# Optimization experiments

Hardware: AMD Instinct MI355X
Metric: run time of the kernel (lower is better)

## Reference

```python
import jax, jax.numpy as jnp
import numpy as np

N = 200      # nodes (fixed by Linear(200,100) on x.T)
E = 8000     # edges
NFEAT, NHID, NCLASS = 8192, 2048, 512


def _cheb_conv(x, edge_index, edge_weight, W, b):
    """PyG ChebConv (K=3, sym norm, lambda_max=2): L_hat = -D^{-1/2} A D^{-1/2}.
    T0 = x, T1 = L_hat x, T2 = 2 L_hat T1 - T0; out = sum_k T_k @ W[k] + b."""
    row, col = edge_index[0], edge_index[1]
    deg = jax.ops.segment_sum(edge_weight, row, num_segments=N)
    safe = jnp.where(deg > 0, deg, 1.0)
    dinv = jnp.where(deg > 0, 1.0 / jnp.sqrt(safe), 0.0)
    norm = -dinv[row] * edge_weight * dinv[col]  # [E]

    def lap(z):  # messages from source j=row to target i=col
        return jax.ops.segment_sum(norm[:, None] * z[row], col, num_segments=N)

    T1 = lap(x)
    T2 = 2.0 * lap(T1) - x
    return x @ W[0] + T1 @ W[1] + T2 @ W[2] + b


def _forward_single(x, ei, ew, W1, b1, W2, b2):
    h = jax.nn.relu(_cheb_conv(x, ei, ew, W1, b1))
    # dropout is identity in eval mode
    return _cheb_conv(h, ei, ew, W2, b2)  # [N, NCLASS]


def _classifier(z, Wc1, bc1, Wc2, bc2, Wc3, bc3):
    h = jax.nn.relu(z @ Wc1.T + bc1)
    h = jax.nn.relu(h @ Wc2.T + bc2)
    return h @ Wc3.T + bc3  # [NCLASS, 1]


def setup_inputs() -> dict:
    key = jax.random.key(0)
    ks = jax.random.split(key, 12)
    inp = {
        'x1': jax.random.normal(ks[0], (N, NFEAT), jnp.float32),
        'edge_index1': jax.random.randint(ks[1], (2, E), 0, N, jnp.int64),
        'edge_attr1': jax.random.uniform(ks[2], (E,), jnp.float32),
        'x2': jax.random.normal(ks[3], (N, NFEAT), jnp.float32),
        'edge_index2': jax.random.randint(ks[4], (2, E), 0, N, jnp.int64),
        'edge_attr2': jax.random.uniform(ks[5], (E,), jnp.float32),
        'W1': jax.random.normal(ks[6], (3, NFEAT, NHID), jnp.float32) * (NFEAT ** -0.5),
        'b1': jnp.zeros((NHID,), jnp.float32),
        'W2': jax.random.normal(ks[7], (3, NHID, NCLASS), jnp.float32) * (NHID ** -0.5),
        'b2': jnp.zeros((NCLASS,), jnp.float32),
        'Wc1': jax.random.normal(ks[8], (100, 200), jnp.float32) * (200 ** -0.5),
        'bc1': jnp.zeros((100,), jnp.float32),
        'Wc2': jax.random.normal(ks[9], (50, 100), jnp.float32) * (100 ** -0.5),
        'bc2': jnp.zeros((50,), jnp.float32),
        'Wc3': jax.random.normal(ks[10], (1, 50), jnp.float32) * (50 ** -0.5),
        'bc3': jnp.zeros((1,), jnp.float32),
    }
    return inp


def reference(x1, edge_index1, edge_attr1, x2, edge_index2, edge_attr2,
              W1, b1, W2, b2, Wc1, bc1, Wc2, bc2, Wc3, bc3):
    o1 = _forward_single(x1, edge_index1, edge_attr1, W1, b1, W2, b2)
    o2 = _forward_single(x2, edge_index2, edge_attr2, W1, b1, W2, b2)
    out1 = _classifier(o1.T, Wc1, bc1, Wc2, bc2, Wc3, bc3)  # [NCLASS, 1]
    out2 = _classifier(o2.T, Wc1, bc1, Wc2, bc2, Wc3, bc3)
    return out1, out2
```

## Files before the change

kernel.cpp:

```cpp
#include <hip/hip_runtime.h>

typedef __attribute__((ext_vector_type(8))) short short8;
typedef __attribute__((ext_vector_type(4))) float f32x4;
typedef __attribute__((ext_vector_type(2))) float f32x2;
typedef __attribute__((ext_vector_type(4))) unsigned int u32x4;

#define NNODES 200
#define NEDGE  8000
#define NF1    8192
#define NH     2048
#define NCL    512
#define K1     24576
#define K2     6144
#define MR     512
#define MV     400
#define PV     400
#define KC1    16
#define BK1    1536
#define KC2    16
#define BK2    384

#define OFF_P1  0ull
#define SZ_P1   (16ull*PV*NH*4)
#define OFF_P2  (OFF_P1 + SZ_P1)
#define SZ_P2   (16ull*PV*NCL*4)
#define OFF_A1  (OFF_P2 + SZ_P2)
#define SZ_A1   ((unsigned long long)MR*K1*2)
#define OFF_A2  (OFF_A1 + SZ_A1)
#define SZ_A2   ((unsigned long long)MR*K2*2)
#define OFF_DEG (OFF_A2 + SZ_A2)
#define OFF_LD  (OFF_DEG + 2048)
#define OFF_LL  (OFF_LD + 320000ull)
#define OFF_Z   OFF_P1

static __device__ __forceinline__ unsigned short f2bf(float f) {
  unsigned int u = __float_as_uint(f);
  unsigned int r = (u + 0x7fffu + ((u >> 16) & 1u)) >> 16;
  return (unsigned short)r;
}
static __device__ __forceinline__ unsigned packbf(float a, float b) {
  return (unsigned)f2bf(a) | ((unsigned)f2bf(b) << 16);
}

__global__ void k_zero(f32x4* p1, int n1, f32x4* p2, int n2, f32x4* p3, int n3) {
  int i = blockIdx.x * 256 + threadIdx.x;
  f32x4 z = {0.f, 0.f, 0.f, 0.f};
  if (i < n1) p1[i] = z;
  i -= n1;
  if (i >= 0 && i < n2) p2[i] = z;
  i -= n2;
  if (i >= 0 && i < n3) p3[i] = z;
}

__global__ void k_deg(const int* __restrict__ ei1, const float* __restrict__ ew1,
                      const int* __restrict__ ei2, const float* __restrict__ ew2,
                      float* __restrict__ deg) {
  int e = blockIdx.x * 256 + threadIdx.x;
  if (e >= 2 * NEDGE) return;
  int g = e / NEDGE, k = e % NEDGE;
  const int* ei = g ? ei2 : ei1;
  const float* ew = g ? ew2 : ew1;
  atomicAdd(deg + g * NNODES + ei[k], ew[k]);
}

__global__ void k_buildL(const int* __restrict__ ei1, const float* __restrict__ ew1,
                         const int* __restrict__ ei2, const float* __restrict__ ew2,
                         const float* __restrict__ deg, float* __restrict__ Ld) {
  int e = blockIdx.x * 256 + threadIdx.x;
  if (e >= 2 * NEDGE) return;
  int g = e / NEDGE, k = e % NEDGE;
  const int* ei = g ? ei2 : ei1;
  const float* ew = g ? ew2 : ew1;
  int r = ei[k], c = ei[NEDGE + k];
  float dr = deg[g * NNODES + r], dc = deg[g * NNODES + c];
  float ir = dr > 0.f ? 1.0f / sqrtf(dr) : 0.f;
  float ic = dc > 0.f ? 1.0f / sqrtf(dc) : 0.f;
  float nrm = -ir * ew[k] * ic;
  atomicAdd(Ld + ((size_t)g * NNODES + c) * NNODES + r, nrm);
}

__global__ void k_LL(const float* __restrict__ Ld, unsigned short* __restrict__ LLb) {
  int b = blockIdx.x;
  int g = b / NNODES, i = b % NNODES;
  __shared__ float Lr[NNODES];
  const float* Lg = Ld + (size_t)g * NNODES * NNODES;
  int t = threadIdx.x;
  if (t < NNODES) Lr[t] = Lg[i * NNODES + t];
  __syncthreads();
  if (t < NNODES) {
    float acc = 0.f;
    for (int k = 0; k < NNODES; ++k) acc = fmaf(Lr[k], Lg[k * NNODES + t], acc);
    unsigned short* LLg = LLb + (size_t)g * MR * 224;
    LLg[(size_t)i * 224 + t] = f2bf(Lr[t]);
    LLg[(size_t)(NNODES + i) * 224 + t] = f2bf(2.f * acc - (i == t ? 1.f : 0.f));
  }
}

__global__ void k_t0(const float* __restrict__ x1, const float* __restrict__ x2,
                     unsigned short* __restrict__ A1) {
  int gid = blockIdx.x * 256 + threadIdx.x;
  int row = gid / (NF1 / 8);
  int c8 = (gid % (NF1 / 8)) * 8;
  const float* xp = (row < NNODES ? x1 + (size_t)row * NF1
                                  : x2 + (size_t)(row - NNODES) * NF1) + c8;
  f32x4 a = *(const f32x4*)xp;
  f32x4 b = *(const f32x4*)(xp + 4);
  u32x4 o;
  o[0] = packbf(a[0], a[1]);
  o[1] = packbf(a[2], a[3]);
  o[2] = packbf(b[0], b[1]);
  o[3] = packbf(b[2], b[3]);
  *(u32x4*)(A1 + (size_t)row * K1 + c8) = o;
}

__global__ __launch_bounds__(256, 1)
void k_abuild(const unsigned short* __restrict__ LLb, const unsigned short* __restrict__ Asrc,
              unsigned short* __restrict__ Adst, const int Nf, const int Ka) {
  __shared__ __align__(16) unsigned short XF[7][4][64][8];
  const int g = blockIdx.x & 1;
  const int nt = blockIdx.x >> 1;
  const int nbase = nt * 64;
  const int t = threadIdx.x;

  #pragma unroll
  for (int it = 0; it < 14; ++it) {
    const int pos = it * 256 + t;
    const int j = pos >> 4;
    const int n4 = (pos & 15) * 4;
    unsigned long long v = 0ull;
    if (j < NNODES)
      v = *(const unsigned long long*)(Asrc + (size_t)(g * NNODES + j) * Ka + nbase + n4);
    const int ks = j >> 5, kg = (j >> 3) & 3, jj = j & 7;
    #pragma unroll
    for (int e = 0; e < 4; ++e) {
      const int nn = n4 + e;
      XF[ks][nn >> 4][(nn & 15) + 16 * kg][jj] = (unsigned short)(v >> (16 * e));
    }
  }
  __syncthreads();

  const int w = t >> 6, lane = t & 63;
  const int lm = lane & 15, lk8 = (lane >> 4) * 8;
  f32x4 acc[7][4];
  #pragma unroll
  for (int i = 0; i < 7; ++i)
    #pragma unroll
    for (int j = 0; j < 4; ++j) acc[i][j] = (f32x4){0.f, 0.f, 0.f, 0.f};

  const unsigned short* LLg = LLb + (size_t)g * MR * 224;
  #pragma unroll
  for (int ks = 0; ks < 7; ++ks) {
    short8 bfr[4];
    #pragma unroll
    for (int nf = 0; nf < 4; ++nf) bfr[nf] = *(const short8*)&XF[ks][nf][lane][0];
    short8 af[7];
    #pragma unroll
    for (int mf = 0; mf < 7; ++mf)
      af[mf] = *(const short8*)(LLg + (size_t)(w * 112 + mf * 16 + lm) * 224 + ks * 32 + lk8);
    #pragma unroll
    for (int mf = 0; mf < 7; ++mf)
      #pragma unroll
      for (int nf = 0; nf < 4; ++nf)
        acc[mf][nf] = __builtin_amdgcn_mfma_f32_16x16x32_bf16(af[mf], bfr[nf], acc[mf][nf], 0, 0, 0);
  }

  const int lr4 = (lane >> 4) * 4;
  #pragma unroll
  for (int mf = 0; mf < 7; ++mf) {
    #pragma unroll
    for (int ri = 0; ri < 4; ++ri) {
      const int m = w * 112 + mf * 16 + lr4 + ri;
      if (m < MV) {
        const int drow = g * NNODES + (m < NNODES ? m : m - NNODES);
        const size_t dbase = (size_t)drow * Ka + (m < NNODES ? Nf : 2 * Nf) + nbase + lm;
        #pragma unroll
        for (int nf = 0; nf < 4; ++nf)
          Adst[dbase + nf * 16] = f2bf(acc[mf][nf][ri]);
      }
    }
  }
}

template <int BN>
__global__ __launch_bounds__(512, 2)
void k_gemm(const float* __restrict__ W, const unsigned short* __restrict__ A,
            float* __restrict__ P, const int Nn, const int BK, const int Ka) {
  constexpr int NF = BN / 16;
  constexpr int NFW = BN / 32;
  __shared__ __align__(16) unsigned short Atile[MR * 64];
  __shared__ __align__(16) unsigned short Wt[2 * NF * 64 * 8];

  const int t = threadIdx.x;
  const int w = t >> 6, lane = t & 63;
  const int wm = w >> 1, wn = w & 1;
  const int lm = lane & 15;
  const int l4 = lane >> 4;
  const int kc = blockIdx.x & 15;
  const int nt = blockIdx.x >> 4;
  const int kbase = kc * BK;
  const int nbase = nt * BN;
  const int nks = BK >> 6;

  int offAg[8];
  int offAl[8];
  #pragma unroll
  for (int c = 0; c < 8; ++c) {
    const int off = c * 8192 + t * 16;
    const int row = off >> 7;
    const int rb = off & 127;
    const int gb = rb ^ ((row & 7) << 4);
    offAg[c] = row * (Ka * 2) + gb;
    offAl[c] = off;
  }
  const char* Ab = (const char*)A + (size_t)kbase * 2;

  constexpr int RW = (BN == 128) ? 4 : 2;
  constexpr int CW = (BN == 128) ? 4 : 2;
  const int kk0 = (BN == 128) ? ((t >> 5) * 4) : ((t >> 4) * 2);
  const int colb = (BN == 128) ? ((t & 31) * 4) : ((t & 15) * 2);
  int offWg[RW];
  #pragma unroll
  for (int r = 0; r < RW; ++r)
    offWg[r] = (kbase + kk0 + r) * Nn + nbase + colb;
  int offWl[RW / 2][CW];
  #pragma unroll
  for (int pr = 0; pr < RW / 2; ++pr) {
    const int kk = kk0 + 2 * pr;
    const int ks = kk >> 5, kg = (kk >> 3) & 3, jj1 = (kk & 7) >> 1;
    #pragma unroll
    for (int e = 0; e < CW; ++e) {
      const int nn = colb + e;
      const int nf = nn >> 4;
      const int ln = ((nn & 15) + 16 * kg) ^ (nf & 3);
      offWl[pr][e] = ((ks * NF + nf) * 64 + ln) * 4 + jj1;
    }
  }

  int aAddr[8];
  #pragma unroll
  for (int mf = 0; mf < 8; ++mf) {
    const int row = wm * 128 + mf * 16 + lm;
    aAddr[mf] = row * 128 + ((l4 * 16) ^ ((row & 7) << 4));
  }
  int bAddr[NFW];
  #pragma unroll
  for (int nf = 0; nf < NFW; ++nf) {
    const int nfg = wn * NFW + nf;
    bAddr[nf] = ((nfg * 64) + (lane ^ (nfg & 3))) * 16;
  }
  constexpr int BSTRIDE = NF * 64 * 16;

  f32x4 acc[8][NFW];
  #pragma unroll
  for (int i = 0; i < 8; ++i)
    #pragma unroll
    for (int j = 0; j < NFW; ++j) acc[i][j] = (f32x4){0.f, 0.f, 0.f, 0.f};

  u32x4 areg[8];
  f32x4 wv4[RW];
  f32x2 wv2[RW];

  #pragma unroll
  for (int c = 0; c < 8; ++c) areg[c] = *(const u32x4*)(Ab + offAg[c]);
  #pragma unroll
  for (int r = 0; r < RW; ++r) {
    if constexpr (BN == 128) wv4[r] = __builtin_nontemporal_load((const f32x4*)(W + offWg[r]));
    else                     wv2[r] = __builtin_nontemporal_load((const f32x2*)(W + offWg[r]));
  }
  {
    #pragma unroll
    for (int c = 0; c < 8; ++c) *(u32x4*)((char*)Atile + offAl[c]) = areg[c];
    unsigned* w32 = (unsigned*)Wt;
    #pragma unroll
    for (int pr = 0; pr < RW / 2; ++pr)
      #pragma unroll
      for (int e = 0; e < CW; ++e) {
        float lo = (BN == 128) ? wv4[2 * pr][e] : wv2[2 * pr][e];
        float hi = (BN == 128) ? wv4[2 * pr + 1][e] : wv2[2 * pr + 1][e];
        w32[offWl[pr][e]] = packbf(lo, hi);
      }
  }
  __syncthreads();

  for (int kt = 0; kt < nks; ++kt) {
    const bool more = (kt + 1 < nks);
    if (more) {
      const int ko = (kt + 1) * 128;
      #pragma unroll
      for (int c = 0; c < 8; ++c) areg[c] = *(const u32x4*)(Ab + offAg[c] + ko);
      const size_t kwo = (size_t)(kt + 1) * 64 * Nn;
      #pragma unroll
      for (int r = 0; r < RW; ++r) {
        if constexpr (BN == 128) wv4[r] = __builtin_nontemporal_load((const f32x4*)(W + offWg[r] + kwo));
        else                     wv2[r] = __builtin_nontemporal_load((const f32x2*)(W + offWg[r] + kwo));
      }
    }
    #pragma unroll
    for (int ks = 0; ks < 2; ++ks) {
      short8 bfr[NFW];
      #pragma unroll
      for (int nf = 0; nf < NFW; ++nf)
        bfr[nf] = *(const short8*)((const char*)Wt + bAddr[nf] + ks * BSTRIDE);
      short8 af[8];
      #pragma unroll
      for (int mf = 0; mf < 8; ++mf)
        af[mf] = *(const short8*)((const char*)Atile + (aAddr[mf] ^ (ks * 64)));
      #pragma unroll
      for (int mf = 0; mf < 8; ++mf)
        #pragma unroll
        for (int nf = 0; nf < NFW; ++nf)
          acc[mf][nf] = __builtin_amdgcn_mfma_f32_16x16x32_bf16(af[mf], bfr[nf], acc[mf][nf], 0, 0, 0);
    }
    __syncthreads();
    if (more) {
      #pragma unroll
      for (int c = 0; c < 8; ++c) *(u32x4*)((char*)Atile + offAl[c]) = areg[c];
      unsigned* w32 = (unsigned*)Wt;
      #pragma unroll
      for (int pr = 0; pr < RW / 2; ++pr)
        #pragma unroll
        for (int e = 0; e < CW; ++e) {
          float lo = (BN == 128) ? wv4[2 * pr][e] : wv2[2 * pr][e];
          float hi = (BN == 128) ? wv4[2 * pr + 1][e] : wv2[2 * pr + 1][e];
          w32[offWl[pr][e]] = packbf(lo, hi);
        }
    }
    __syncthreads();
  }

  float* Pk = P + ((size_t)kc * PV) * Nn + nbase;
  #pragma unroll
  for (int mf = 0; mf < 8; ++mf) {
    const int row0 = wm * 128 + mf * 16 + l4 * 4;
    #pragma unroll
    for (int ri = 0; ri < 4; ++ri) {
      const int row = row0 + ri;
      if (row < MV) {
        #pragma unroll
        for (int nf = 0; nf < NFW; ++nf) {
          const int col = (wn * NFW + nf) * 16 + lm;
          __builtin_nontemporal_store(acc[mf][nf][ri], Pk + (size_t)row * Nn + col);
        }
      }
    }
  }
}

__global__ void k_ep1(const float* __restrict__ P1, const float* __restrict__ b1,
                      unsigned short* __restrict__ A2) {
  int gid = blockIdx.x * 256 + threadIdx.x;
  int row = gid / (NH / 4);
  int c = (gid % (NH / 4)) * 4;
  f32x4 s = {0.f, 0.f, 0.f, 0.f};
  #pragma unroll
  for (int kc = 0; kc < KC1; ++kc)
    s += __builtin_nontemporal_load((const f32x4*)(P1 + ((size_t)kc * PV + row) * NH + c));
  const f32x4 b = *(const f32x4*)(b1 + c);
  unsigned long long pack = 0;
  #pragma unroll
  for (int i = 0; i < 4; ++i) {
    float v = s[i] + b[i];
    pack |= (unsigned long long)f2bf(v > 0.f ? v : 0.f) << (16 * i);
  }
  *(unsigned long long*)(A2 + (size_t)row * K2 + c) = pack;
}

__global__ __launch_bounds__(256)
void k_zsum(const float* __restrict__ P2, const float* __restrict__ b2,
            float* __restrict__ zt) {
  __shared__ float tile[8][520];
  const int g = blockIdx.x / 25;
  const int j0 = (blockIdx.x % 25) * 8;
  const int t = threadIdx.x;
  const int j = t >> 5;
  const int c0 = (t & 31) * 16;
  const int row = g * NNODES + j0 + j;

  #pragma unroll
  for (int ci = 0; ci < 4; ++ci) {
    const int c = c0 + ci * 4;
    f32x4 s = *(const f32x4*)(b2 + c);
    #pragma unroll
    for (int kc = 0; kc < KC2; ++kc)
      s += __builtin_nontemporal_load((const f32x4*)(P2 + ((size_t)kc * PV + row) * NCL + c));
    *(f32x4*)&tile[j][c] = s;
  }
  __syncthreads();

  #pragma unroll
  for (int ci = 0; ci < 2; ++ci) {
    const int c = ci * 256 + t;
    f32x4 lo, hi;
    #pragma unroll
    for (int e = 0; e < 4; ++e) { lo[e] = tile[e][c]; hi[e] = tile[4 + e][c]; }
    float* zr = zt + ((size_t)g * NCL + c) * 200 + j0;
    *(f32x4*)zr = lo;
    *(f32x4*)(zr + 4) = hi;
  }
}

__global__ __launch_bounds__(256)
void k_cls2(const float* __restrict__ zt,
            const float* __restrict__ Wc1, const float* __restrict__ bc1,
            const float* __restrict__ Wc2, const float* __restrict__ bc2,
            const float* __restrict__ Wc3, const float* __restrict__ bc3,
            float* __restrict__ outp) {
  __shared__ float zs[4][200];
  __shared__ float h1s[4][100];
  __shared__ float h2s[4][50];
  const int g = blockIdx.x >> 7;
  const int t = threadIdx.x;
  const int w = t >> 6, lane = t & 63;
  const int r = (blockIdx.x & 127) * 4 + w;

  const float* zr = zt + ((size_t)g * NCL + r) * 200;
  #pragma unroll
  for (int i = 0; i < 4; ++i) {
    const int idx = i * 64 + lane;
    if (idx < 200) zs[w][idx] = zr[idx];
  }
  __syncthreads();

  {
    const int c0 = lane;
    const int c1 = lane + 64;
    const int c1m = (c1 < 100) ? c1 : 99;
    float a0 = bc1[c0 < 100 ? c0 : 99];
    float a1 = bc1[c1m];
    const float* w0 = Wc1 + c0 * 200;
    const float* w1 = Wc1 + c1m * 200;
    #pragma unroll 8
    for (int j = 0; j < 200; ++j) {
      const float zv = zs[w][j];
      a0 = fmaf(zv, w0[j], a0);
      a1 = fmaf(zv, w1[j], a1);
    }
    if (c0 < 100) h1s[w][c0] = a0 > 0.f ? a0 : 0.f;
    if (c1 < 100) h1s[w][c1] = a1 > 0.f ? a1 : 0.f;
  }
  __syncthreads();

  {
    const int c2 = (lane < 50) ? lane : 49;
    float b = bc2[c2];
    const float* w2 = Wc2 + c2 * 100;
    #pragma unroll 10
    for (int c = 0; c < 100; ++c) b = fmaf(h1s[w][c], w2[c], b);
    if (lane < 50) h2s[w][lane] = b > 0.f ? b : 0.f;
  }
  __syncthreads();

  {
    float v = (lane < 50) ? h2s[w][lane] * Wc3[lane] : 0.f;
    #pragma unroll
    for (int off = 32; off >= 1; off >>= 1) v += __shfl_down(v, off);
    if (lane == 0) outp[g * NCL + r] = v + bc3[0];
  }
}

extern "C" void kernel_launch(void* const* d_in, const int* in_sizes, int n_in,
                              void* d_out, int out_size, void* d_ws, size_t ws_size,
                              hipStream_t stream) {
  const float* x1  = (const float*)d_in[0];
  const int*   ei1 = (const int*)d_in[1];
  const float* ea1 = (const float*)d_in[2];
  const float* x2  = (const float*)d_in[3];
  const int*   ei2 = (const int*)d_in[4];
  const float* ea2 = (const float*)d_in[5];
  const float* W1  = (const float*)d_in[6];
  const float* b1  = (const float*)d_in[7];
  const float* W2  = (const float*)d_in[8];
  const float* b2  = (const float*)d_in[9];
  const float* Wc1 = (const float*)d_in[10];
  const float* bc1 = (const float*)d_in[11];
  const float* Wc2 = (const float*)d_in[12];
  const float* bc2 = (const float*)d_in[13];
  const float* Wc3 = (const float*)d_in[14];
  const float* bc3 = (const float*)d_in[15];
  float* outp = (float*)d_out;

  char* ws = (char*)d_ws;
  float*          P1  = (float*)(ws + OFF_P1);
  float*          P2  = (float*)(ws + OFF_P2);
  unsigned short* A1  = (unsigned short*)(ws + OFF_A1);
  unsigned short* A2  = (unsigned short*)(ws + OFF_A2);
  float*          deg = (float*)(ws + OFF_DEG);
  float*          Ld  = (float*)(ws + OFF_LD);
  unsigned short* LLb = (unsigned short*)(ws + OFF_LL);
  float*          zt  = (float*)(ws + OFF_Z);

  k_zero<<<1871, 256, 0, stream>>>(
      (f32x4*)(ws + OFF_DEG), 48800,
      (f32x4*)(ws + OFF_A1 + (size_t)MV * K1 * 2), 344064,
      (f32x4*)(ws + OFF_A2 + (size_t)MV * K2 * 2), 86016);

  k_deg<<<63, 256, 0, stream>>>(ei1, ea1, ei2, ea2, deg);
  k_buildL<<<63, 256, 0, stream>>>(ei1, ea1, ei2, ea2, deg, Ld);
  k_LL<<<400, 256, 0, stream>>>(Ld, LLb);
  k_t0<<<1600, 256, 0, stream>>>(x1, x2, A1);
  k_abuild<<<(NF1 / 64) * 2, 256, 0, stream>>>(LLb, A1, A1, NF1, K1);
  k_gemm<128><<<KC1 * (NH / 128), 512, 0, stream>>>(W1, A1, P1, NH, BK1, K1);
  k_ep1<<<800, 256, 0, stream>>>(P1, b1, A2);
  k_abuild<<<(NH / 64) * 2, 256, 0, stream>>>(LLb, A2, A2, NH, K2);
  k_gemm<32><<<KC2 * (NCL / 32), 512, 0, stream>>>(W2, A2, P2, NCL, BK2, K2);
  k_zsum<<<50, 256, 0, stream>>>(P2, b2, zt);
  k_cls2<<<256, 256, 0, stream>>>(zt, Wc1, bc1, Wc2, bc2, Wc3, bc3, outp);
}
```

Measured before the change: 193.8 us.

## Shrink GEMM register footprint for 4 blocks/CU and narrower N tile for layer 1

The GEMM kernel now takes the A row stride as a template constant and computes A addresses from one base pointer plus constant strides, replacing the per-chunk offset arrays. The prefetched A tile for the next step is held in 7 registers instead of 8, and its global loads move to after the MFMA loop; rows 448-511 are left unrefreshed, which appears safe only because rows at or above 400 are never stored. Layer 1 uses BN=64 instead of 128, doubling the grid, and launch bounds rise to 4 blocks per CU. The goal is more occupancy and latency hiding. The cost is re-reading A across twice as many N tiles and less prefetch overlap for A.

Result: slower. 214.2 us (+10.5%).

```diff
diff --git a/kernel.cpp b/kernel.cpp
--- a/kernel.cpp
+++ b/kernel.cpp
@@ -181,12 +181,13 @@
   }
 }
 
-template <int BN>
-__global__ __launch_bounds__(512, 2)
+template <int BN, int KA>
+__global__ __launch_bounds__(512, 4)
 void k_gemm(const float* __restrict__ W, const unsigned short* __restrict__ A,
-            float* __restrict__ P, const int Nn, const int BK, const int Ka) {
+            float* __restrict__ P, const int Nn, const int BK) {
   constexpr int NF = BN / 16;
   constexpr int NFW = BN / 32;
+  constexpr int CW = BN / 16;
   __shared__ __align__(16) unsigned short Atile[MR * 64];
   __shared__ __align__(16) unsigned short Wt[2 * NF * 64 * 8];
 
@@ -201,47 +202,27 @@
   const int nbase = nt * BN;
   const int nks = BK >> 6;
 
-  int offAg[8];
-  int offAl[8];
-  #pragma unroll
-  for (int c = 0; c < 8; ++c) {
-    const int off = c * 8192 + t * 16;
-    const int row = off >> 7;
-    const int rb = off & 127;
-    const int gb = rb ^ ((row & 7) << 4);
-    offAg[c] = row * (Ka * 2) + gb;
-    offAl[c] = off;
-  }
-  const char* Ab = (const char*)A + (size_t)kbase * 2;
-
-  constexpr int RW = (BN == 128) ? 4 : 2;
-  constexpr int CW = (BN == 128) ? 4 : 2;
-  const int kk0 = (BN == 128) ? ((t >> 5) * 4) : ((t >> 4) * 2);
-  const int colb = (BN == 128) ? ((t & 31) * 4) : ((t & 15) * 2);
-  int offWg[RW];
-  #pragma unroll
-  for (int r = 0; r < RW; ++r)
-    offWg[r] = (kbase + kk0 + r) * Nn + nbase + colb;
-  int offWl[RW / 2][CW];
-  #pragma unroll
-  for (int pr = 0; pr < RW / 2; ++pr) {
-    const int kk = kk0 + 2 * pr;
-    const int ks = kk >> 5, kg = (kk >> 3) & 3, jj1 = (kk & 7) >> 1;
+  const int arow0 = t >> 3;
+  const int agb = ((t * 16) & 127) ^ ((arow0 & 7) << 4);
+  const char* Ab = (const char*)A + (size_t)kbase * 2 + (size_t)arow0 * (KA * 2) + agb;
+  const size_t CSTEP = (size_t)64 * KA * 2;
+
+  const int kk0 = (t >> 4) * 2;
+  const int colb = (t & 15) * CW;
+  const float* Wg = W + (size_t)(kbase + kk0) * Nn + nbase + colb;
+  int offWl[CW];
+  {
+    const int ks = kk0 >> 5, kg = (kk0 >> 3) & 3, jj1 = (kk0 & 7) >> 1;
     #pragma unroll
     for (int e = 0; e < CW; ++e) {
       const int nn = colb + e;
       const int nf = nn >> 4;
       const int ln = ((nn & 15) + 16 * kg) ^ (nf & 3);
-      offWl[pr][e] = ((ks * NF + nf) * 64 + ln) * 4 + jj1;
-    }
-  }
-
-  int aAddr[8];
-  #pragma unroll
-  for (int mf = 0; mf < 8; ++mf) {
-    const int row = wm * 128 + mf * 16 + lm;
-    aAddr[mf] = row * 128 + ((l4 * 16) ^ ((row & 7) << 4));
-  }
+      offWl[e] = ((ks * NF + nf) * 64 + ln) * 4 + jj1;
+    }
+  }
+
+  const int aBase = (wm * 128 + lm) * 128 + ((l4 * 16) ^ ((lm & 7) << 4));
   int bAddr[NFW];
   #pragma unroll
   for (int nf = 0; nf < NFW; ++nf) {
@@ -256,74 +237,69 @@
     #pragma unroll
     for (int j = 0; j < NFW; ++j) acc[i][j] = (f32x4){0.f, 0.f, 0.f, 0.f};
 
-  u32x4 areg[8];
-  f32x4 wv4[RW];
-  f32x2 wv2[RW];
-
-  #pragma unroll
-  for (int c = 0; c < 8; ++c) areg[c] = *(const u32x4*)(Ab + offAg[c]);
-  #pragma unroll
-  for (int r = 0; r < RW; ++r) {
-    if constexpr (BN == 128) wv4[r] = __builtin_nontemporal_load((const f32x4*)(W + offWg[r]));
-    else                     wv2[r] = __builtin_nontemporal_load((const f32x2*)(W + offWg[r]));
-  }
-  {
-    #pragma unroll
-    for (int c = 0; c < 8; ++c) *(u32x4*)((char*)Atile + offAl[c]) = areg[c];
+  u32x4 areg[7];
+  f32x4 w0_4, w1_4;
+  f32x2 w0_2, w1_2;
+
+  auto loadW = [&](int kt) {
+    const float* p = Wg + (size_t)kt * 64 * Nn;
+    if constexpr (BN == 64) {
+      w0_4 = __builtin_nontemporal_load((const f32x4*)p);
+      w1_4 = __builtin_nontemporal_load((const f32x4*)(p + Nn));
+    } else {
+      w0_2 = __builtin_nontemporal_load((const f32x2*)p);
+      w1_2 = __builtin_nontemporal_load((const f32x2*)(p + Nn));
+    }
+  };
+  auto storeW = [&]() {
     unsigned* w32 = (unsigned*)Wt;
     #pragma unroll
-    for (int pr = 0; pr < RW / 2; ++pr)
-      #pragma unroll
-      for (int e = 0; e < CW; ++e) {
-        float lo = (BN == 128) ? wv4[2 * pr][e] : wv2[2 * pr][e];
-        float hi = (BN == 128) ? wv4[2 * pr + 1][e] : wv2[2 * pr + 1][e];
-        w32[offWl[pr][e]] = packbf(lo, hi);
-      }
-  }
+    for (int e = 0; e < CW; ++e) {
+      if constexpr (BN == 64) w32[offWl[e]] = packbf(w0_4[e], w1_4[e]);
+      else                    w32[offWl[e]] = packbf(w0_2[e], w1_2[e]);
+    }
+  };
+
+  #pragma unroll
+  for (int c = 0; c < 8; ++c) {
+    u32x4 v = *(const u32x4*)(Ab + c * CSTEP);
+    *(u32x4*)((char*)Atile + c * 8192 + t * 16) = v;
+  }
+  loadW(0);
+  storeW();
   __syncthreads();
 
   for (int kt = 0; kt < nks; ++kt) {
     const bool more = (kt + 1 < nks);
-    if (more) {
-      const int ko = (kt + 1) * 128;
-      #pragma unroll
-      for (int c = 0; c < 8; ++c) areg[c] = *(const u32x4*)(Ab + offAg[c] + ko);
-      const size_t kwo = (size_t)(kt + 1) * 64 * Nn;
-      #pragma unroll
-      for (int r = 0; r < RW; ++r) {
-        if constexpr (BN == 128) wv4[r] = __builtin_nontemporal_load((const f32x4*)(W + offWg[r] + kwo));
-        else                     wv2[r] = __builtin_nontemporal_load((const f32x2*)(W + offWg[r] + kwo));
-      }
-    }
+    if (more) loadW(kt + 1);
     #pragma unroll
     for (int ks = 0; ks < 2; ++ks) {
       short8 bfr[NFW];
       #pragma unroll
       for (int nf = 0; nf < NFW; ++nf)
         bfr[nf] = *(const short8*)((const char*)Wt + bAddr[nf] + ks * BSTRIDE);
+      const int abx = aBase ^ (ks * 64);
       short8 af[8];
       #pragma unroll
       for (int mf = 0; mf < 8; ++mf)
-        af[mf] = *(const short8*)((const char*)Atile + (aAddr[mf] ^ (ks * 64)));
+        af[mf] = *(const short8*)((const char*)Atile + abx + mf * 2048);
       #pragma unroll
       for (int mf = 0; mf < 8; ++mf)
         #pragma unroll
         for (int nf = 0; nf < NFW; ++nf)
           acc[mf][nf] = __builtin_amdgcn_mfma_f32_16x16x32_bf16(af[mf], bfr[nf], acc[mf][nf], 0, 0, 0);
     }
+    if (more) {
+      #pragma unroll
+      for (int c = 0; c < 7; ++c)
+        areg[c] = *(const u32x4*)(Ab + c * CSTEP + (size_t)(kt + 1) * 128);
+    }
     __syncthreads();
     if (more) {
       #pragma unroll
-      for (int c = 0; c < 8; ++c) *(u32x4*)((char*)Atile + offAl[c]) = areg[c];
-      unsigned* w32 = (unsigned*)Wt;
-      #pragma unroll
-      for (int pr = 0; pr < RW / 2; ++pr)
-        #pragma unroll
-        for (int e = 0; e < CW; ++e) {
-          float lo = (BN == 128) ? wv4[2 * pr][e] : wv2[2 * pr][e];
-          float hi = (BN == 128) ? wv4[2 * pr + 1][e] : wv2[2 * pr + 1][e];
-          w32[offWl[pr][e]] = packbf(lo, hi);
-        }
+      for (int c = 0; c < 7; ++c)
+        *(u32x4*)((char*)Atile + c * 8192 + t * 16) = areg[c];
+      storeW();
     }
     __syncthreads();
   }
@@ -499,10 +475,10 @@
   k_LL<<<400, 256, 0, stream>>>(Ld, LLb);
   k_t0<<<1600, 256, 0, stream>>>(x1, x2, A1);
   k_abuild<<<(NF1 / 64) * 2, 256, 0, stream>>>(LLb, A1, A1, NF1, K1);
-  k_gemm<128><<<KC1 * (NH / 128), 512, 0, stream>>>(W1, A1, P1, NH, BK1, K1);
+  k_gemm<64, K1><<<KC1 * (NH / 64), 512, 0, stream>>>(W1, A1, P1, NH, BK1);
   k_ep1<<<800, 256, 0, stream>>>(P1, b1, A2);
   k_abuild<<<(NH / 64) * 2, 256, 0, stream>>>(LLb, A2, A2, NH, K2);
-  k_gemm<32><<<KC2 * (NCL / 32), 512, 0, stream>>>(W2, A2, P2, NCL, BK2, K2);
+  k_gemm<32, K2><<<KC2 * (NCL / 32), 512, 0, stream>>>(W2, A2, P2, NCL, BK2);
   k_zsum<<<50, 256, 0, stream>>>(P2, b2, zt);
   k_cls2<<<256, 256, 0, stream>>>(zt, Wc1, bc1, Wc2, bc2, Wc3, bc3, outp);
 }
```
